# Kernel optimization log

Hardware: AMD Instinct MI355X
Metric: run time of the kernel (lower is better)

## Reference

```python
import math
import jax, jax.numpy as jnp
import numpy as np

B, T, D, H = 4, 1024, 1024, 8
DK = D // H
SCALE = 1.0 / math.sqrt(DK)
NEG_INF = -10000.0
P = 2 * T - 1


def setup_inputs() -> dict:
    key = jax.random.key(0)
    ks = jax.random.split(key, 16)
    s = 0.02
    return {
        "query": jax.random.normal(ks[0], (B, T, D), jnp.float32),
        "key": jax.random.normal(ks[1], (B, T, D), jnp.float32),
        "value": jax.random.normal(ks[2], (B, T, D), jnp.float32),
        "pos_emb": jax.random.normal(ks[3], (1, P, D), jnp.float32),
        "mask": jnp.zeros((B, T, T), dtype=bool),  # True = masked
        "Wq": jax.random.normal(ks[4], (D, D), jnp.float32) * s,
        "bq": jax.random.normal(ks[5], (D,), jnp.float32) * s,
        "Wk": jax.random.normal(ks[6], (D, D), jnp.float32) * s,
        "bk": jax.random.normal(ks[7], (D,), jnp.float32) * s,
        "Wv": jax.random.normal(ks[8], (D, D), jnp.float32) * s,
        "bv": jax.random.normal(ks[9], (D,), jnp.float32) * s,
        "Wp": jax.random.normal(ks[10], (D, D), jnp.float32) * s,  # linear_pos, no bias
        "Wo": jax.random.normal(ks[11], (D, D), jnp.float32) * s,
        "bo": jax.random.normal(ks[12], (D,), jnp.float32) * s,
        "pos_bias_u": jax.random.normal(ks[13], (H, DK), jnp.float32) * s,
        "pos_bias_v": jax.random.normal(ks[14], (H, DK), jnp.float32) * s,
    }


def _rel_shift(x):
    # x: (B, H, T, P) with P = 2T-1. Transformer-XL skewing trick.
    b, h, qlen, pos_len = x.shape
    x = jnp.pad(x, ((0, 0), (0, 0), (0, 0), (1, 0)))
    x = x.reshape(b, h, pos_len + 1, qlen)
    x = x[:, :, 1:].reshape(b, h, qlen, pos_len)
    return x


def reference(query, key, value, pos_emb, mask, Wq, bq, Wk, bk, Wv, bv, Wp, Wo, bo,
              pos_bias_u, pos_bias_v):
    b, t, _ = query.shape
    q = (query @ Wq + bq).reshape(b, t, H, DK)          # (B,T,H,dk)
    k = (key @ Wk + bk).reshape(b, t, H, DK).transpose(0, 2, 1, 3)   # (B,H,T,dk)
    v = (value @ Wv + bv).reshape(b, t, H, DK).transpose(0, 2, 1, 3)

    pos_len = pos_emb.shape[1]
    p = (pos_emb @ Wp).reshape(pos_len, H, DK).transpose(1, 0, 2)    # (H,P,dk)

    q_u = (q + pos_bias_u).transpose(0, 2, 1, 3)        # (B,H,T,dk)
    q_v = (q + pos_bias_v).transpose(0, 2, 1, 3)

    # position-bias scores: (B,H,T,P)
    matrix_bd = jnp.einsum('bhtd,hpd->bhtp', q_v, p)
    matrix_bd = _rel_shift(matrix_bd)[:, :, :, :t] * SCALE           # (B,H,T,T)
    m = mask[:, None]                                   # (B,1,T,T)
    matrix_bd = jnp.where(m, NEG_INF, matrix_bd)

    # SDPA with additive mask: softmax(QK^T*scale + bd) @ V
    scores = jnp.einsum('bhtd,bhsd->bhts', q_u, k) * SCALE + matrix_bd
    attn = jax.nn.softmax(scores, axis=-1)
    out = jnp.einsum('bhts,bhsd->bhtd', attn, v)        # (B,H,T,dk)

    all_masked = jnp.all(m, axis=-1)[..., None]         # (B,1,T,1)
    out = jnp.where(all_masked, 0.0, out)

    out = out.transpose(0, 2, 1, 3).reshape(b, t, D)
    return out @ Wo + bo
```

## Files before the change

kernel.cpp:

```cpp
#include <hip/hip_runtime.h>
#include <cstddef>


#define B_ 4
#define T_ 1024
#define D_ 1024
#define H_ 8
#define DK_ 128
#define P_ 2047
#define SCALE_F 0.08838834764831845f
#define NEG_INF_F (-10000.0f)

typedef unsigned short ushort_t;
typedef __attribute__((ext_vector_type(8))) short short8;
typedef __attribute__((ext_vector_type(8))) unsigned short ushortx8;
typedef __attribute__((ext_vector_type(4))) float f32x4;

__device__ __forceinline__ ushort_t f2bf(float f) {
    unsigned u = __float_as_uint(f);
    unsigned r = (u + 0x7FFFu + ((u >> 16) & 1u)) >> 16;
    return (ushort_t)r;
}
__device__ __forceinline__ float bf2f(ushort_t b) {
    return __uint_as_float(((unsigned)b) << 16);
}

__device__ __forceinline__ void gload_lds16(const ushort_t* src, ushort_t* dst) {
    __builtin_amdgcn_global_load_lds(
        (const __attribute__((address_space(1))) unsigned int*)src,
        (__attribute__((address_space(3))) unsigned int*)dst, 16, 0, 0);
}

__device__ __forceinline__ void stage128x64(const ushort_t* __restrict__ g, int ldg,
                                            int rowBase, int rowMax,
                                            ushort_t* lds, int k0)
{
    const int tid = threadIdx.x;
    const int w = tid >> 6;
    #pragma unroll
    for (int u = 0; u < 4; ++u) {
        int e = tid * 8 + u * 2048;
        int row = e >> 6, col = e & 63;
        int gr = rowBase + row; if (gr > rowMax - 1) gr = rowMax - 1;
        const ushort_t* src = g + (size_t)gr * ldg + k0 + col;
        ushort_t* dst = lds + w * 512 + u * 2048;
        gload_lds16(src, dst);
    }
}

__device__ __forceinline__ void mma128(const ushort_t* As, const ushort_t* Bs, f32x4 acc[4][4])
{
    const int lane = threadIdx.x & 63;
    const int w = threadIdx.x >> 6;
    const int wr = (w >> 1) * 64, wc = (w & 1) * 64;
    const int lr = lane & 15, lk = (lane >> 4) * 8;
    #pragma unroll
    for (int kk = 0; kk < 2; ++kk) {
        short8 a[4], b[4];
        #pragma unroll
        for (int i = 0; i < 4; ++i)
            a[i] = *(const short8*)&As[(size_t)(wr + i * 16 + lr) * 64 + kk * 32 + lk];
        #pragma unroll
        for (int j = 0; j < 4; ++j)
            b[j] = *(const short8*)&Bs[(size_t)(wc + j * 16 + lr) * 64 + kk * 32 + lk];
        #pragma unroll
        for (int i = 0; i < 4; ++i)
            #pragma unroll
            for (int j = 0; j < 4; ++j)
                acc[i][j] = __builtin_amdgcn_mfma_f32_16x16x32_bf16(a[i], b[j], acc[i][j], 0, 0, 0);
    }
}

#define ACC_DECL f32x4 acc[4][4]; \
    _Pragma("unroll") for (int i_ = 0; i_ < 4; ++i_) \
    _Pragma("unroll") for (int j_ = 0; j_ < 4; ++j_) \
    _Pragma("unroll") for (int r_ = 0; r_ < 4; ++r_) acc[i_][j_][r_] = 0.f;

#define EPI_COORDS \
    const int lane = threadIdx.x & 63; \
    const int w = threadIdx.x >> 6; \
    const int wr = (w >> 1) * 64, wc = (w & 1) * 64; \
    const int lcol = lane & 15, lrow4 = (lane >> 4) * 4;

template<int MODE>
__global__ __launch_bounds__(256)
void gemm_proj_bt(const ushort_t* __restrict__ A, const ushort_t* __restrict__ Bt,
                  const float* __restrict__ bias,
                  void* __restrict__ out0, void* __restrict__ out1,
                  const float* __restrict__ pbu, const float* __restrict__ pbv, int M)
{
    __shared__ ushort_t As[128 * 64], Bs[128 * 64];
    const int n0 = blockIdx.x * 128, m0 = blockIdx.y * 128;
    ACC_DECL;
    for (int k0 = 0; k0 < 1024; k0 += 64) {
        stage128x64(A, 1024, m0, M, As, k0);
        stage128x64(Bt, 1024, n0, 1024, Bs, k0);
        __syncthreads();
        mma128(As, Bs, acc);
        __syncthreads();
    }
    EPI_COORDS;
    #pragma unroll
    for (int i = 0; i < 4; ++i)
        #pragma unroll
        for (int j = 0; j < 4; ++j)
            #pragma unroll
            for (int r = 0; r < 4; ++r) {
                int m = m0 + wr + i * 16 + lrow4 + r;
                int n = n0 + wc + j * 16 + lcol;
                if (m >= M) continue;
                float v = acc[i][j][r];
                size_t o = (size_t)m * 1024 + n;
                if (MODE == 0) { ((ushort_t*)out0)[o] = f2bf(v + bias[n]); }
                else if (MODE == 1) {
                    v += bias[n];
                    ((ushort_t*)out0)[o] = f2bf(v + pbu[n]);
                    ((ushort_t*)out1)[o] = f2bf(v + pbv[n]);
                } else if (MODE == 2) { ((float*)out0)[o] = v + bias[n]; }
                else { ((ushort_t*)out0)[o] = f2bf(v); }
            }
}

__global__ __launch_bounds__(256)
void gemm_bd_shifted(const ushort_t* __restrict__ qv, const ushort_t* __restrict__ p,
                     ushort_t* __restrict__ bdS, int b0)
{
    __shared__ ushort_t As[128 * 64], Bs[128 * 64];
    const int j0 = blockIdx.x * 128, t0 = blockIdx.y * 128;
    const int lb = blockIdx.z >> 3, h = blockIdx.z & 7;
    const int b = b0 + lb;
    const ushort_t* Ab = qv + (size_t)b * T_ * D_ + h * DK_;
    const ushort_t* Bb = p + h * DK_;
    ACC_DECL;
    for (int k0 = 0; k0 < DK_; k0 += 64) {
        stage128x64(Ab, D_, t0, T_, As, k0);
        stage128x64(Bb, D_, j0, P_, Bs, k0);
        __syncthreads();
        mma128(As, Bs, acc);
        __syncthreads();
    }
    EPI_COORDS;
    ushort_t* ob = bdS + (size_t)(lb * H_ + h) * T_ * T_;
    #pragma unroll
    for (int i = 0; i < 4; ++i)
        #pragma unroll
        for (int j = 0; j < 4; ++j)
            #pragma unroll
            for (int r = 0; r < 4; ++r) {
                int t = t0 + wr + i * 16 + lrow4 + r;
                int jj = j0 + wc + j * 16 + lcol;
                int s = jj + t - (T_ - 1);
                if (s >= 0 && s < T_)
                    ob[(size_t)t * T_ + s] = f2bf(acc[i][j][r]);
            }
}

__device__ __forceinline__ void stage_swz(const ushort_t* __restrict__ g, int ldg,
                                          int rowBase, ushort_t* lds, int k0)
{
    const int tid = threadIdx.x;
    const int w = tid >> 6;
    #pragma unroll
    for (int u = 0; u < 2; ++u) {
        int e = tid * 8 + u * 4096;
        int row = e >> 6;
        int blk = (e >> 3) & 7;
        const ushort_t* src = g + (size_t)(rowBase + row) * ldg + k0 + ((blk ^ (row & 7)) << 3);
        ushort_t* dst = lds + w * 512 + u * 4096;
        gload_lds16(src, dst);
    }
}

__global__ __launch_bounds__(512, 2)
void flash_attn(const ushort_t* __restrict__ qu, const ushort_t* __restrict__ kb,
                const ushort_t* __restrict__ vT, const ushort_t* __restrict__ bdS,
                const unsigned char* __restrict__ mask,
                ushort_t* __restrict__ ctx, int b0)
{
    __shared__ ushort_t Sb[128 * 64];
    __shared__ ushort_t Sp[2][128 * 64];
    __shared__ float stats_m[4][128];
    __shared__ float stats_l[4][128];

    const int tid = threadIdx.x;
    const int lane = tid & 63, w = tid >> 6;
    const int wr = (w >> 2) * 64, wc = (w & 3) * 32;
    const int wcol = w & 3;
    const int lr = lane & 15;
    const int lg = lane >> 4;
    const int lrow4 = lg * 4;
    const int t0 = blockIdx.x * 128;
    const int lb = blockIdx.y >> 3, h = blockIdx.y & 7;
    const int b = b0 + lb;
    const int spHalf = wc >> 6;

    const ushort_t* quB = qu + (size_t)b * T_ * D_ + h * DK_;
    const ushort_t* kB  = kb + (size_t)b * T_ * D_ + h * DK_;
    const ushort_t* vTB = vT + (size_t)(b * H_ + h) * DK_ * T_;
    const ushort_t* bdB = bdS + (size_t)(lb * H_ + h) * T_ * T_;
    const unsigned char* mB = mask + (size_t)b * T_ * T_;

    f32x4 acc_o[4][2];
    float m_run[4][4], l_run[4][4];
    #pragma unroll
    for (int i = 0; i < 4; ++i) {
        #pragma unroll
        for (int j = 0; j < 2; ++j)
            #pragma unroll
            for (int r = 0; r < 4; ++r) acc_o[i][j][r] = 0.f;
        #pragma unroll
        for (int r = 0; r < 4; ++r) { m_run[i][r] = -3.0e38f; l_run[i][r] = 0.f; }
    }

    for (int s0 = 0; s0 < T_; s0 += 128) {
        f32x4 acc_s[4][2];
        #pragma unroll
        for (int i = 0; i < 4; ++i)
            #pragma unroll
            for (int j = 0; j < 2; ++j)
                #pragma unroll
                for (int r = 0; r < 4; ++r) {
                    int t = t0 + wr + i * 16 + lrow4 + r;
                    int s = s0 + wc + j * 16 + lr;
                    size_t off = (size_t)t * T_ + s;
                    float bdv = bf2f(bdB[off]);
                    acc_s[i][j][r] = mB[off] ? (NEG_INF_F / SCALE_F) : bdv;
                }
        #pragma unroll
        for (int kh = 0; kh < 2; ++kh) {
            __syncthreads();
            stage_swz(kB, D_, s0, Sb, kh * 64);
            short8 aQ[2][4];
            #pragma unroll
            for (int kk = 0; kk < 2; ++kk)
                #pragma unroll
                for (int i = 0; i < 4; ++i)
                    aQ[kk][i] = *(const short8*)&quB[(size_t)(t0 + wr + i * 16 + lr) * D_
                                                     + kh * 64 + kk * 32 + lg * 8];
            __syncthreads();
            #pragma unroll
            for (int kk = 0; kk < 2; ++kk) {
                short8 bf[2];
                #pragma unroll
                for (int j = 0; j < 2; ++j) {
                    int row = wc + j * 16 + lr;
                    bf[j] = *(const short8*)&Sb[row * 64 + (((kk * 4 + lg) ^ (row & 7)) << 3)];
                }
                #pragma unroll
                for (int i = 0; i < 4; ++i)
                    #pragma unroll
                    for (int j = 0; j < 2; ++j)
                        acc_s[i][j] = __builtin_amdgcn_mfma_f32_16x16x32_bf16(
                            aQ[kk][i], bf[j], acc_s[i][j], 0, 0, 0);
            }
        }
        float m_loc[4][4];
        #pragma unroll
        for (int i = 0; i < 4; ++i)
            #pragma unroll
            for (int r = 0; r < 4; ++r) {
                float mv = -3.0e38f;
                #pragma unroll
                for (int j = 0; j < 2; ++j) {
                    float sv = acc_s[i][j][r] * SCALE_F;
                    acc_s[i][j][r] = sv;
                    mv = fmaxf(mv, sv);
                }
                #pragma unroll
                for (int off = 1; off < 16; off <<= 1)
                    mv = fmaxf(mv, __shfl_xor(mv, off));
                m_loc[i][r] = mv;
            }
        if (lr == 0) {
            #pragma unroll
            for (int i = 0; i < 4; ++i)
                #pragma unroll
                for (int r = 0; r < 4; ++r)
                    stats_m[wcol][wr + i * 16 + lrow4 + r] = m_loc[i][r];
        }
        __syncthreads();
        float fsc[4][4];
        #pragma unroll
        for (int i = 0; i < 4; ++i)
            #pragma unroll
            for (int r = 0; r < 4; ++r) {
                int row = wr + i * 16 + lrow4 + r;
                float mt = fmaxf(fmaxf(stats_m[0][row], stats_m[1][row]),
                                 fmaxf(stats_m[2][row], stats_m[3][row]));
                float mn = fmaxf(m_run[i][r], mt);
                fsc[i][r] = __expf(m_run[i][r] - mn);
                m_run[i][r] = mn;
            }
        float ls[4][4];
        #pragma unroll
        for (int i = 0; i < 4; ++i)
            #pragma unroll
            for (int r = 0; r < 4; ++r) {
                float sum = 0.f;
                int row = wr + i * 16 + lrow4 + r;
                #pragma unroll
                for (int j = 0; j < 2; ++j) {
                    float pexp = __expf(acc_s[i][j][r] - m_run[i][r]);
                    sum += pexp;
                    int c = (wc & 63) + j * 16 + lr;
                    int slot = (((c >> 3) ^ (row & 7)) << 3) | (c & 7);
                    Sp[spHalf][row * 64 + slot] = f2bf(pexp);
                }
                #pragma unroll
                for (int off = 1; off < 16; off <<= 1)
                    sum += __shfl_xor(sum, off);
                ls[i][r] = sum;
            }
        if (lr == 0) {
            #pragma unroll
            for (int i = 0; i < 4; ++i)
                #pragma unroll
                for (int r = 0; r < 4; ++r)
                    stats_l[wcol][wr + i * 16 + lrow4 + r] = ls[i][r];
        }
        __syncthreads();
        #pragma unroll
        for (int i = 0; i < 4; ++i)
            #pragma unroll
            for (int r = 0; r < 4; ++r) {
                int row = wr + i * 16 + lrow4 + r;
                float lt = stats_l[0][row] + stats_l[1][row]
                         + stats_l[2][row] + stats_l[3][row];
                l_run[i][r] = l_run[i][r] * fsc[i][r] + lt;
            }
        #pragma unroll
        for (int i = 0; i < 4; ++i)
            #pragma unroll
            for (int j = 0; j < 2; ++j)
                #pragma unroll
                for (int r = 0; r < 4; ++r)
                    acc_o[i][j][r] *= fsc[i][r];
        #pragma unroll
        for (int sh = 0; sh < 2; ++sh) {
            if (sh) __syncthreads();
            stage_swz(vTB, T_, 0, Sb, s0 + sh * 64);
            __syncthreads();
            #pragma unroll
            for (int kk = 0; kk < 2; ++kk) {
                short8 bf[2], af[4];
                #pragma unroll
                for (int j = 0; j < 2; ++j) {
                    int row = wc + j * 16 + lr;
                    bf[j] = *(const short8*)&Sb[row * 64 + (((kk * 4 + lg) ^ (row & 7)) << 3)];
                }
                #pragma unroll
                for (int i = 0; i < 4; ++i) {
                    int rowA = wr + i * 16 + lr;
                    af[i] = *(const short8*)&Sp[sh][rowA * 64 + (((kk * 4 + lg) ^ (rowA & 7)) << 3)];
                }
                #pragma unroll
                for (int i = 0; i < 4; ++i)
                    #pragma unroll
                    for (int j = 0; j < 2; ++j)
                        acc_o[i][j] = __builtin_amdgcn_mfma_f32_16x16x32_bf16(
                            af[i], bf[j], acc_o[i][j], 0, 0, 0);
            }
        }
    }
    #pragma unroll
    for (int i = 0; i < 4; ++i)
        #pragma unroll
        for (int r = 0; r < 4; ++r) {
            float inv = (m_run[i][r] < -5000.f) ? 0.f : 1.f / l_run[i][r];
            #pragma unroll
            for (int j = 0; j < 2; ++j) {
                int t = t0 + wr + i * 16 + lrow4 + r;
                int n = wc + j * 16 + lr;
                ctx[((size_t)(b * T_ + t)) * D_ + h * DK_ + n] = f2bf(acc_o[i][j][r] * inv);
            }
        }
}

__global__ __launch_bounds__(256)
void cast_bf16(const float* __restrict__ in, ushort_t* __restrict__ out, int n)
{
    int i = (blockIdx.x * 256 + threadIdx.x) * 8;
    if (i >= n) return;
    float4 a = *(const float4*)&in[i];
    float4 bq = *(const float4*)&in[i + 4];
    ushortx8 r;
    r[0] = f2bf(a.x); r[1] = f2bf(a.y); r[2] = f2bf(a.z); r[3] = f2bf(a.w);
    r[4] = f2bf(bq.x); r[5] = f2bf(bq.y); r[6] = f2bf(bq.z); r[7] = f2bf(bq.w);
    *(ushortx8*)&out[i] = r;
}

__global__ __launch_bounds__(256)
void wt_cast(const float* __restrict__ W, ushort_t* __restrict__ Wt)
{
    __shared__ float tile[32][33];
    const int n0 = blockIdx.x * 32, k0 = blockIdx.y * 32;
    const int lx = threadIdx.x & 31, ly = threadIdx.x >> 5;
    #pragma unroll
    for (int r = 0; r < 32; r += 8)
        tile[ly + r][lx] = W[(size_t)(k0 + ly + r) * 1024 + n0 + lx];
    __syncthreads();
    #pragma unroll
    for (int r = 0; r < 32; r += 8)
        Wt[(size_t)(n0 + ly + r) * 1024 + k0 + lx] = f2bf(tile[lx][ly + r]);
}

__global__ __launch_bounds__(256)
void vt_trans(const ushort_t* __restrict__ v, ushort_t* __restrict__ vT)
{
    __shared__ ushort_t tile[32][33];
    const int t0 = blockIdx.x * 32, n0 = blockIdx.y * 32;
    const int bh = blockIdx.z;
    const int b = bh >> 3, h = bh & 7;
    const int lx = threadIdx.x & 31, ly = threadIdx.x >> 5;
    const ushort_t* src = v + (size_t)b * T_ * D_ + h * DK_;
    #pragma unroll
    for (int r = 0; r < 32; r += 8)
        tile[ly + r][lx] = src[(size_t)(t0 + ly + r) * D_ + n0 + lx];
    __syncthreads();
    ushort_t* dst = vT + (size_t)bh * DK_ * T_;
    #pragma unroll
    for (int r = 0; r < 32; r += 8)
        dst[(size_t)(n0 + ly + r) * T_ + t0 + lx] = tile[lx][ly + r];
}

extern "C" void kernel_launch(void* const* d_in, const int* in_sizes, int n_in,
                              void* d_out, int out_size, void* d_ws, size_t ws_size,
                              hipStream_t stream)
{
    const float* query   = (const float*)d_in[0];
    const float* key     = (const float*)d_in[1];
    const float* value   = (const float*)d_in[2];
    const float* pos_emb = (const float*)d_in[3];
    const unsigned char* mask = (const unsigned char*)d_in[4];
    const float* Wq  = (const float*)d_in[5];
    const float* bq  = (const float*)d_in[6];
    const float* Wk  = (const float*)d_in[7];
    const float* bk  = (const float*)d_in[8];
    const float* Wv  = (const float*)d_in[9];
    const float* bv  = (const float*)d_in[10];
    const float* Wp  = (const float*)d_in[11];
    const float* Wo  = (const float*)d_in[12];
    const float* bo  = (const float*)d_in[13];
    const float* pbu = (const float*)d_in[14];
    const float* pbv = (const float*)d_in[15];
    float* out = (float*)d_out;

    const size_t SZ_BTD = (size_t)B_ * T_ * D_;
    const size_t SZ_PD  = (size_t)P_ * D_;
    const size_t SZ_W   = (size_t)D_ * D_;

    ushort_t* c = (ushort_t*)d_ws;
    ushort_t* qbf  = c; c += SZ_BTD;
    ushort_t* kbfi = c; c += SZ_BTD;
    ushort_t* vbfi = c; c += SZ_BTD;
    ushort_t* pbf  = c; c += SZ_PD;
    ushort_t* WqT = c; c += SZ_W;
    ushort_t* WkT = c; c += SZ_W;
    ushort_t* WvT = c; c += SZ_W;
    ushort_t* WpT = c; c += SZ_W;
    ushort_t* WoT = c; c += SZ_W;
    ushort_t* qu  = c; c += SZ_BTD;
    ushort_t* qv  = c; c += SZ_BTD;
    ushort_t* kb  = c; c += SZ_BTD;
    ushort_t* vb  = c; c += SZ_BTD;
    ushort_t* ctx = c; c += SZ_BTD;
    ushort_t* vT  = c; c += SZ_BTD;
    ushort_t* pp  = c; c += SZ_PD;

    const size_t base_bytes = (size_t)((char*)c - (char*)d_ws);
    const size_t per_b = (size_t)H_ * T_ * T_ * 2;
    int SB = 1;
    if (ws_size > base_bytes) {
        size_t sb = (ws_size - base_bytes) / per_b;
        SB = sb < 1 ? 1 : (sb > B_ ? B_ : (int)sb);
    }
    ushort_t* bdS = c;

    cast_bf16<<<dim3((int)(SZ_BTD / 8 / 256)), 256, 0, stream>>>(query, qbf, (int)SZ_BTD);
    cast_bf16<<<dim3((int)(SZ_BTD / 8 / 256)), 256, 0, stream>>>(key, kbfi, (int)SZ_BTD);
    cast_bf16<<<dim3((int)(SZ_BTD / 8 / 256)), 256, 0, stream>>>(value, vbfi, (int)SZ_BTD);
    cast_bf16<<<dim3((int)((SZ_PD / 8 + 255) / 256)), 256, 0, stream>>>(pos_emb, pbf, (int)SZ_PD);
    wt_cast<<<dim3(32, 32), 256, 0, stream>>>(Wq, WqT);
    wt_cast<<<dim3(32, 32), 256, 0, stream>>>(Wk, WkT);
    wt_cast<<<dim3(32, 32), 256, 0, stream>>>(Wv, WvT);
    wt_cast<<<dim3(32, 32), 256, 0, stream>>>(Wp, WpT);
    wt_cast<<<dim3(32, 32), 256, 0, stream>>>(Wo, WoT);

    gemm_proj_bt<1><<<dim3(8, 32), 256, 0, stream>>>(qbf, WqT, bq, qu, qv, pbu, pbv, B_ * T_);
    gemm_proj_bt<0><<<dim3(8, 32), 256, 0, stream>>>(kbfi, WkT, bk, kb, nullptr, nullptr, nullptr, B_ * T_);
    gemm_proj_bt<0><<<dim3(8, 32), 256, 0, stream>>>(vbfi, WvT, bv, vb, nullptr, nullptr, nullptr, B_ * T_);
    gemm_proj_bt<3><<<dim3(8, 16), 256, 0, stream>>>(pbf, WpT, nullptr, pp, nullptr, nullptr, nullptr, P_);
    vt_trans<<<dim3(32, 4, 32), 256, 0, stream>>>(vb, vT);

    for (int b0 = 0; b0 < B_; b0 += SB) {
        int nb = B_ - b0; if (nb > SB) nb = SB;
        gemm_bd_shifted<<<dim3(16, 8, nb * H_), 256, 0, stream>>>(qv, pp, bdS, b0);
        flash_attn     <<<dim3(8, nb * H_),     512, 0, stream>>>(qu, kb, vT, bdS, mask, ctx, b0);
    }

    gemm_proj_bt<2><<<dim3(8, 32), 256, 0, stream>>>(ctx, WoT, bo, (void*)out, nullptr, nullptr, nullptr, B_ * T_);
}
```

Before: 480.8 us.

## Batch QKVP projections, fold mask into bd, shrink attention tile with LDS-staged bias

The four input projections now run as one launch with a z-dimension selecting Q/K/V/P, and the output projection gets its own kernel. The mask is applied in the bd-score epilogue, so flash attention no longer reads the byte mask per element. Flash attention moves from 128-row, 512-thread blocks to 64-row, 256-thread blocks with three blocks per CU. Each bd tile is loaded into LDS with async global-to-LDS copies instead of scattered per-lane global loads, and the V staging is overlapped with the softmax. The trade-off is more blocks, fewer waves per block, and extra LDS use per block.

```diff
diff --git a/kernel.cpp b/kernel.cpp
--- a/kernel.cpp
+++ b/kernel.cpp
@@ -82,13 +82,24 @@
     const int wr = (w >> 1) * 64, wc = (w & 1) * 64; \
     const int lcol = lane & 15, lrow4 = (lane >> 4) * 4;
 
-template<int MODE>
 __global__ __launch_bounds__(256)
-void gemm_proj_bt(const ushort_t* __restrict__ A, const ushort_t* __restrict__ Bt,
-                  const float* __restrict__ bias,
-                  void* __restrict__ out0, void* __restrict__ out1,
-                  const float* __restrict__ pbu, const float* __restrict__ pbv, int M)
-{
+void gemm_qkvp(const ushort_t* __restrict__ qA, const ushort_t* __restrict__ kA,
+               const ushort_t* __restrict__ vA, const ushort_t* __restrict__ pA,
+               const ushort_t* __restrict__ WqT, const ushort_t* __restrict__ WkT,
+               const ushort_t* __restrict__ WvT, const ushort_t* __restrict__ WpT,
+               const float* __restrict__ bq, const float* __restrict__ bk,
+               const float* __restrict__ bv,
+               ushort_t* __restrict__ quO, ushort_t* __restrict__ qvO,
+               ushort_t* __restrict__ kO, ushort_t* __restrict__ vO,
+               ushort_t* __restrict__ pO,
+               const float* __restrict__ pbu, const float* __restrict__ pbv)
+{
+    const int z = blockIdx.z;
+    if (z == 3 && blockIdx.y >= 16) return;
+    const ushort_t* A  = z == 0 ? qA  : z == 1 ? kA  : z == 2 ? vA  : pA;
+    const ushort_t* Bt = z == 0 ? WqT : z == 1 ? WkT : z == 2 ? WvT : WpT;
+    const int M = (z == 3) ? P_ : B_ * T_;
+
     __shared__ ushort_t As[128 * 64], Bs[128 * 64];
     const int n0 = blockIdx.x * 128, m0 = blockIdx.y * 128;
     ACC_DECL;
@@ -111,18 +122,47 @@
                 if (m >= M) continue;
                 float v = acc[i][j][r];
                 size_t o = (size_t)m * 1024 + n;
-                if (MODE == 0) { ((ushort_t*)out0)[o] = f2bf(v + bias[n]); }
-                else if (MODE == 1) {
-                    v += bias[n];
-                    ((ushort_t*)out0)[o] = f2bf(v + pbu[n]);
-                    ((ushort_t*)out1)[o] = f2bf(v + pbv[n]);
-                } else if (MODE == 2) { ((float*)out0)[o] = v + bias[n]; }
-                else { ((ushort_t*)out0)[o] = f2bf(v); }
+                if (z == 0) {
+                    v += bq[n];
+                    quO[o] = f2bf(v + pbu[n]);
+                    qvO[o] = f2bf(v + pbv[n]);
+                } else if (z == 1) kO[o] = f2bf(v + bk[n]);
+                else if (z == 2)  vO[o] = f2bf(v + bv[n]);
+                else              pO[o] = f2bf(v);
+            }
+}
+
+__global__ __launch_bounds__(256)
+void gemm_out(const ushort_t* __restrict__ A, const ushort_t* __restrict__ Bt,
+              const float* __restrict__ bias, float* __restrict__ out, int M)
+{
+    __shared__ ushort_t As[128 * 64], Bs[128 * 64];
+    const int n0 = blockIdx.x * 128, m0 = blockIdx.y * 128;
+    ACC_DECL;
+    for (int k0 = 0; k0 < 1024; k0 += 64) {
+        stage128x64(A, 1024, m0, M, As, k0);
+        stage128x64(Bt, 1024, n0, 1024, Bs, k0);
+        __syncthreads();
+        mma128(As, Bs, acc);
+        __syncthreads();
+    }
+    EPI_COORDS;
+    #pragma unroll
+    for (int i = 0; i < 4; ++i)
+        #pragma unroll
+        for (int j = 0; j < 4; ++j)
+            #pragma unroll
+            for (int r = 0; r < 4; ++r) {
+                int m = m0 + wr + i * 16 + lrow4 + r;
+                int n = n0 + wc + j * 16 + lcol;
+                if (m >= M) continue;
+                out[(size_t)m * 1024 + n] = acc[i][j][r] + bias[n];
             }
 }
 
 __global__ __launch_bounds__(256)
 void gemm_bd_shifted(const ushort_t* __restrict__ qv, const ushort_t* __restrict__ p,
+                     const unsigned char* __restrict__ mask,
                      ushort_t* __restrict__ bdS, int b0)
 {
     __shared__ ushort_t As[128 * 64], Bs[128 * 64];
@@ -140,7 +180,9 @@
         __syncthreads();
     }
     EPI_COORDS;
+    const ushort_t MASKED_BF = f2bf(NEG_INF_F / SCALE_F);
     ushort_t* ob = bdS + (size_t)(lb * H_ + h) * T_ * T_;
+    const unsigned char* mB = mask + (size_t)b * T_ * T_;
     #pragma unroll
     for (int i = 0; i < 4; ++i)
         #pragma unroll
@@ -150,55 +192,54 @@
                 int t = t0 + wr + i * 16 + lrow4 + r;
                 int jj = j0 + wc + j * 16 + lcol;
                 int s = jj + t - (T_ - 1);
-                if (s >= 0 && s < T_)
-                    ob[(size_t)t * T_ + s] = f2bf(acc[i][j][r]);
-            }
-}
-
-__device__ __forceinline__ void stage_swz(const ushort_t* __restrict__ g, int ldg,
-                                          int rowBase, ushort_t* lds, int k0)
+                if (s >= 0 && s < T_) {
+                    unsigned char mk = mB[(size_t)t * T_ + s];
+                    ob[(size_t)t * T_ + s] = mk ? MASKED_BF : f2bf(acc[i][j][r]);
+                }
+            }
+}
+
+__device__ __forceinline__ void stage_swz256(const ushort_t* __restrict__ g, int ldg,
+                                             int rowBase, ushort_t* lds, int k0)
 {
     const int tid = threadIdx.x;
     const int w = tid >> 6;
     #pragma unroll
-    for (int u = 0; u < 2; ++u) {
-        int e = tid * 8 + u * 4096;
+    for (int u = 0; u < 4; ++u) {
+        int e = tid * 8 + u * 2048;
         int row = e >> 6;
         int blk = (e >> 3) & 7;
         const ushort_t* src = g + (size_t)(rowBase + row) * ldg + k0 + ((blk ^ (row & 7)) << 3);
-        ushort_t* dst = lds + w * 512 + u * 4096;
+        ushort_t* dst = lds + w * 512 + u * 2048;
         gload_lds16(src, dst);
     }
 }
 
-__global__ __launch_bounds__(512, 2)
+__global__ __launch_bounds__(256, 3)
 void flash_attn(const ushort_t* __restrict__ qu, const ushort_t* __restrict__ kb,
                 const ushort_t* __restrict__ vT, const ushort_t* __restrict__ bdS,
-                const unsigned char* __restrict__ mask,
                 ushort_t* __restrict__ ctx, int b0)
 {
     __shared__ ushort_t Sb[128 * 64];
-    __shared__ ushort_t Sp[2][128 * 64];
-    __shared__ float stats_m[4][128];
-    __shared__ float stats_l[4][128];
+    __shared__ ushort_t Sp[64 * 128];
+    __shared__ ushort_t Sd[64 * 128];
+    __shared__ float stats_m[4][64];
+    __shared__ float stats_l[4][64];
 
     const int tid = threadIdx.x;
     const int lane = tid & 63, w = tid >> 6;
-    const int wr = (w >> 2) * 64, wc = (w & 3) * 32;
-    const int wcol = w & 3;
+    const int wc = w * 32;
     const int lr = lane & 15;
     const int lg = lane >> 4;
     const int lrow4 = lg * 4;
-    const int t0 = blockIdx.x * 128;
+    const int t0 = blockIdx.x * 64;
     const int lb = blockIdx.y >> 3, h = blockIdx.y & 7;
     const int b = b0 + lb;
-    const int spHalf = wc >> 6;
 
     const ushort_t* quB = qu + (size_t)b * T_ * D_ + h * DK_;
     const ushort_t* kB  = kb + (size_t)b * T_ * D_ + h * DK_;
     const ushort_t* vTB = vT + (size_t)(b * H_ + h) * DK_ * T_;
     const ushort_t* bdB = bdS + (size_t)(lb * H_ + h) * T_ * T_;
-    const unsigned char* mB = mask + (size_t)b * T_ * T_;
 
     f32x4 acc_o[4][2];
     float m_run[4][4], l_run[4][4];
@@ -213,31 +254,39 @@
     }
 
     for (int s0 = 0; s0 < T_; s0 += 128) {
+        __syncthreads();
+        #pragma unroll
+        for (int u = 0; u < 4; ++u) {
+            int e = tid * 8 + u * 2048;
+            int row = e >> 7, col = e & 127;
+            gload_lds16(bdB + (size_t)(t0 + row) * T_ + s0 + col, Sd + w * 512 + u * 2048);
+        }
+        stage_swz256(kB, D_, s0, Sb, 0);
+        __syncthreads();
+
         f32x4 acc_s[4][2];
         #pragma unroll
         for (int i = 0; i < 4; ++i)
             #pragma unroll
             for (int j = 0; j < 2; ++j)
                 #pragma unroll
-                for (int r = 0; r < 4; ++r) {
-                    int t = t0 + wr + i * 16 + lrow4 + r;
-                    int s = s0 + wc + j * 16 + lr;
-                    size_t off = (size_t)t * T_ + s;
-                    float bdv = bf2f(bdB[off]);
-                    acc_s[i][j][r] = mB[off] ? (NEG_INF_F / SCALE_F) : bdv;
-                }
+                for (int r = 0; r < 4; ++r)
+                    acc_s[i][j][r] = bf2f(Sd[(i * 16 + lrow4 + r) * 128 + wc + j * 16 + lr]);
+
         #pragma unroll
         for (int kh = 0; kh < 2; ++kh) {
-            __syncthreads();
-            stage_swz(kB, D_, s0, Sb, kh * 64);
+            if (kh) {
+                __syncthreads();
+                stage_swz256(kB, D_, s0, Sb, 64);
+                __syncthreads();
+            }
             short8 aQ[2][4];
             #pragma unroll
             for (int kk = 0; kk < 2; ++kk)
                 #pragma unroll
                 for (int i = 0; i < 4; ++i)
-                    aQ[kk][i] = *(const short8*)&quB[(size_t)(t0 + wr + i * 16 + lr) * D_
+                    aQ[kk][i] = *(const short8*)&quB[(size_t)(t0 + i * 16 + lr) * D_
                                                      + kh * 64 + kk * 32 + lg * 8];
-            __syncthreads();
             #pragma unroll
             for (int kk = 0; kk < 2; ++kk) {
                 short8 bf[2];
@@ -254,7 +303,7 @@
                             aQ[kk][i], bf[j], acc_s[i][j], 0, 0, 0);
             }
         }
-        float m_loc[4][4];
+
         #pragma unroll
         for (int i = 0; i < 4; ++i)
             #pragma unroll
@@ -269,64 +318,49 @@
                 #pragma unroll
                 for (int off = 1; off < 16; off <<= 1)
                     mv = fmaxf(mv, __shfl_xor(mv, off));
-                m_loc[i][r] = mv;
-            }
-        if (lr == 0) {
-            #pragma unroll
-            for (int i = 0; i < 4; ++i)
-                #pragma unroll
-                for (int r = 0; r < 4; ++r)
-                    stats_m[wcol][wr + i * 16 + lrow4 + r] = m_loc[i][r];
-        }
-        __syncthreads();
+                if (lr == 0) stats_m[w][i * 16 + lrow4 + r] = mv;
+            }
+        __syncthreads();
+        stage_swz256(vTB, T_, 0, Sb, s0);
         float fsc[4][4];
         #pragma unroll
         for (int i = 0; i < 4; ++i)
             #pragma unroll
             for (int r = 0; r < 4; ++r) {
-                int row = wr + i * 16 + lrow4 + r;
+                int row = i * 16 + lrow4 + r;
                 float mt = fmaxf(fmaxf(stats_m[0][row], stats_m[1][row]),
                                  fmaxf(stats_m[2][row], stats_m[3][row]));
                 float mn = fmaxf(m_run[i][r], mt);
                 fsc[i][r] = __expf(m_run[i][r] - mn);
                 m_run[i][r] = mn;
             }
-        float ls[4][4];
         #pragma unroll
         for (int i = 0; i < 4; ++i)
             #pragma unroll
             for (int r = 0; r < 4; ++r) {
                 float sum = 0.f;
-                int row = wr + i * 16 + lrow4 + r;
+                int row = i * 16 + lrow4 + r;
                 #pragma unroll
                 for (int j = 0; j < 2; ++j) {
                     float pexp = __expf(acc_s[i][j][r] - m_run[i][r]);
                     sum += pexp;
-                    int c = (wc & 63) + j * 16 + lr;
-                    int slot = (((c >> 3) ^ (row & 7)) << 3) | (c & 7);
-                    Sp[spHalf][row * 64 + slot] = f2bf(pexp);
+                    int c = wc + j * 16 + lr;
+                    Sp[row * 128 + ((((c >> 3) ^ (row & 7)) << 3) | (c & 7))] = f2bf(pexp);
                 }
                 #pragma unroll
                 for (int off = 1; off < 16; off <<= 1)
                     sum += __shfl_xor(sum, off);
-                ls[i][r] = sum;
-            }
-        if (lr == 0) {
-            #pragma unroll
-            for (int i = 0; i < 4; ++i)
-                #pragma unroll
-                for (int r = 0; r < 4; ++r)
-                    stats_l[wcol][wr + i * 16 + lrow4 + r] = ls[i][r];
-        }
-        __syncthreads();
-        #pragma unroll
-        for (int i = 0; i < 4; ++i)
-            #pragma unroll
-            for (int r = 0; r < 4; ++r) {
-                int row = wr + i * 16 + lrow4 + r;
-                float lt = stats_l[0][row] + stats_l[1][row]
-                         + stats_l[2][row] + stats_l[3][row];
-                l_run[i][r] = l_run[i][r] * fsc[i][r] + lt;
+                if (lr == 0) stats_l[w][row] = sum;
+            }
+        __syncthreads();
+        #pragma unroll
+        for (int i = 0; i < 4; ++i)
+            #pragma unroll
+            for (int r = 0; r < 4; ++r) {
+                int row = i * 16 + lrow4 + r;
+                l_run[i][r] = l_run[i][r] * fsc[i][r]
+                            + stats_l[0][row] + stats_l[1][row]
+                            + stats_l[2][row] + stats_l[3][row];
             }
         #pragma unroll
         for (int i = 0; i < 4; ++i)
@@ -335,11 +369,14 @@
                 #pragma unroll
                 for (int r = 0; r < 4; ++r)
                     acc_o[i][j][r] *= fsc[i][r];
+
         #pragma unroll
         for (int sh = 0; sh < 2; ++sh) {
-            if (sh) __syncthreads();
-            stage_swz(vTB, T_, 0, Sb, s0 + sh * 64);
-            __syncthreads();
+            if (sh) {
+                __syncthreads();
+                stage_swz256(vTB, T_, 0, Sb, s0 + 64);
+                __syncthreads();
+            }
             #pragma unroll
             for (int kk = 0; kk < 2; ++kk) {
                 short8 bf[2], af[4];
@@ -350,8 +387,9 @@
                 }
                 #pragma unroll
                 for (int i = 0; i < 4; ++i) {
-                    int rowA = wr + i * 16 + lr;
-                    af[i] = *(const short8*)&Sp[sh][rowA * 64 + (((kk * 4 + lg) ^ (rowA & 7)) << 3)];
+                    int rowA = i * 16 + lr;
+                    int cb = sh * 8 + kk * 4 + lg;
+                    af[i] = *(const short8*)&Sp[rowA * 128 + ((cb ^ (rowA & 7)) << 3)];
                 }
                 #pragma unroll
                 for (int i = 0; i < 4; ++i)
@@ -362,6 +400,7 @@
             }
         }
     }
+
     #pragma unroll
     for (int i = 0; i < 4; ++i)
         #pragma unroll
@@ -369,7 +408,7 @@
             float inv = (m_run[i][r] < -5000.f) ? 0.f : 1.f / l_run[i][r];
             #pragma unroll
             for (int j = 0; j < 2; ++j) {
-                int t = t0 + wr + i * 16 + lrow4 + r;
+                int t = t0 + i * 16 + lrow4 + r;
                 int n = wc + j * 16 + lr;
                 ctx[((size_t)(b * T_ + t)) * D_ + h * DK_ + n] = f2bf(acc_o[i][j][r] * inv);
             }
@@ -486,17 +525,17 @@
     wt_cast<<<dim3(32, 32), 256, 0, stream>>>(Wp, WpT);
     wt_cast<<<dim3(32, 32), 256, 0, stream>>>(Wo, WoT);
 
-    gemm_proj_bt<1><<<dim3(8, 32), 256, 0, stream>>>(qbf, WqT, bq, qu, qv, pbu, pbv, B_ * T_);
-    gemm_proj_bt<0><<<dim3(8, 32), 256, 0, stream>>>(kbfi, WkT, bk, kb, nullptr, nullptr, nullptr, B_ * T_);
-    gemm_proj_bt<0><<<dim3(8, 32), 256, 0, stream>>>(vbfi, WvT, bv, vb, nullptr, nullptr, nullptr, B_ * T_);
-    gemm_proj_bt<3><<<dim3(8, 16), 256, 0, stream>>>(pbf, WpT, nullptr, pp, nullptr, nullptr, nullptr, P_);
+    gemm_qkvp<<<dim3(8, 32, 4), 256, 0, stream>>>(qbf, kbfi, vbfi, pbf,
+                                                  WqT, WkT, WvT, WpT,
+                                                  bq, bk, bv,
+                                                  qu, qv, kb, vb, pp, pbu, pbv);
     vt_trans<<<dim3(32, 4, 32), 256, 0, stream>>>(vb, vT);
 
     for (int b0 = 0; b0 < B_; b0 += SB) {
         int nb = B_ - b0; if (nb > SB) nb = SB;
-        gemm_bd_shifted<<<dim3(16, 8, nb * H_), 256, 0, stream>>>(qv, pp, bdS, b0);
-        flash_attn     <<<dim3(8, nb * H_),     512, 0, stream>>>(qu, kb, vT, bdS, mask, ctx, b0);
-    }
-
-    gemm_proj_bt<2><<<dim3(8, 32), 256, 0, stream>>>(ctx, WoT, bo, (void*)out, nullptr, nullptr, nullptr, B_ * T_);
-}
+        gemm_bd_shifted<<<dim3(16, 8, nb * H_), 256, 0, stream>>>(qv, pp, mask, bdS, b0);
+        flash_attn     <<<dim3(16, nb * H_),    256, 0, stream>>>(qu, kb, vT, bdS, ctx, b0);
+    }
+
+    gemm_out<<<dim3(8, 32), 256, 0, stream>>>(ctx, WoT, bo, out, B_ * T_);
+}
```

Measured after the change: 659.4 us. +37.1%, slower.
